# Kernel optimization log

Hardware: AMD Instinct MI355X
Metric: run time of the kernel (lower is better)

## Reference

```python
import jax, jax.numpy as jnp
import numpy as np

DIM = 1024
NUM_HEADS = 16
HEAD_DIM = DIM // NUM_HEADS


def _rope_tables(seq_len, dim, dtype):
    # matches llama_rotary_embedding: inv_freq over even indices of head_dim
    inv_freq = 1.0 / (10000.0 ** (jnp.arange(0, dim, 2, dtype=jnp.float32) / dim))
    t = jnp.arange(seq_len, dtype=jnp.float32)
    freqs = jnp.outer(t, inv_freq)  # [S, dim/2]
    return jnp.cos(freqs).astype(dtype), jnp.sin(freqs).astype(dtype)


def _apply_rope(x, cos_emb, sin_emb):
    # x: [B, H, S, hd]; takes interleaved halves, concatenates rotated halves
    x1 = x[..., 0::2]
    x2 = x[..., 1::2]
    return jnp.concatenate((x1 * cos_emb - x2 * sin_emb,
                            x1 * sin_emb + x2 * cos_emb), axis=-1)


def setup_inputs() -> dict:
    key = jax.random.key(0)
    k_x, k_qkv, k_out, k_b = jax.random.split(key, 4)
    B, S, D = 2, 2048, DIM
    x = jax.random.normal(k_x, (B, S, D), dtype=jnp.float32)
    # torch nn.Linear weights are [out_features, in_features]
    w_qkv = jax.random.normal(k_qkv, (3 * D, D), dtype=jnp.float32) * (1.0 / np.sqrt(D))
    w_out = jax.random.normal(k_out, (D, D), dtype=jnp.float32) * (1.0 / np.sqrt(D))
    b_out = jax.random.normal(k_b, (D,), dtype=jnp.float32) * 0.01
    return {"x": x, "w_qkv": w_qkv, "w_out": w_out, "b_out": b_out}


def reference(x, w_qkv, w_out, b_out):
    B, S, D = x.shape
    H, hd = NUM_HEADS, HEAD_DIM
    qkv = jnp.einsum('bsd,ed->bse', x, w_qkv)  # [B, S, 3D]
    q, k, v = jnp.split(qkv, 3, axis=-1)
    # [B, S, D] -> [B, H, S, hd]
    q, k, v = (t.reshape(B, S, H, hd).transpose(0, 2, 1, 3) for t in (q, k, v))
    cos_emb, sin_emb = _rope_tables(S, hd, x.dtype)  # [S, hd/2]
    q = _apply_rope(q, cos_emb, sin_emb)
    k = _apply_rope(k, cos_emb, sin_emb)
    scores = jnp.einsum('bhqd,bhkd->bhqk', q, k) / jnp.sqrt(jnp.asarray(hd, x.dtype))
    attn = jax.nn.softmax(scores, axis=-1)
    out = jnp.einsum('bhqk,bhkd->bhqd', attn, v)
    out = out.transpose(0, 2, 1, 3).reshape(B, S, D)
    return jnp.einsum('bsd,ed->bse', out, w_out) + b_out
```

## Files before the change

### kernel.cpp

```cpp
#include <hip/hip_runtime.h>
#include <math.h>

typedef __bf16 bf16_t;
typedef bf16_t bf16x8 __attribute__((ext_vector_type(8)));
typedef bf16_t bf16x4 __attribute__((ext_vector_type(4)));
typedef short  s16x4  __attribute__((ext_vector_type(4)));
typedef float  f32x4  __attribute__((ext_vector_type(4)));

#define DIM_   1024
#define NHEADS 16
#define HDIM   64
#define SEQ    2048
#define BATCH  2

#define QK_SCALE 0.18033688011112042f

__device__ __forceinline__ s16x4 as_s16x4(bf16x4 v) {
    union { bf16x4 b; s16x4 s; } u; u.b = v; return u.s;
}

__device__ __forceinline__ void gld16(const bf16_t* g, bf16_t* l) {
    __builtin_amdgcn_global_load_lds(
        (const __attribute__((address_space(1))) void*)g,
        (__attribute__((address_space(3))) void*)l, 16, 0, 0);
}

#define XCNT   (4096u * 1024u)
#define WQCNT  (3072u * 1024u)
#define WOCNT  (1024u * 1024u)
__global__ __launch_bounds__(256) void cast3(const float* __restrict__ s0,
                                             const float* __restrict__ s1,
                                             const float* __restrict__ s2,
                                             bf16_t* __restrict__ d0,
                                             bf16_t* __restrict__ d1,
                                             bf16_t* __restrict__ d2) {
    size_t i = ((size_t)blockIdx.x * 256 + threadIdx.x) * 8;
    const float* s; bf16_t* d; size_t off;
    if (i < XCNT)               { s = s0; d = d0; off = i; }
    else if (i < XCNT + WQCNT)  { s = s1; d = d1; off = i - XCNT; }
    else                        { s = s2; d = d2; off = i - XCNT - WQCNT; }
    float4 a = *(const float4*)(s + off);
    float4 b = *(const float4*)(s + off + 4);
    bf16x8 o = { (bf16_t)a.x, (bf16_t)a.y, (bf16_t)a.z, (bf16_t)a.w,
                 (bf16_t)b.x, (bf16_t)b.y, (bf16_t)b.z, (bf16_t)b.w };
    *(bf16x8*)(d + off) = o;
}

template <bool QKV>
__global__ __launch_bounds__(256) void gemm_lds(const bf16_t* __restrict__ A,
                                                const bf16_t* __restrict__ B,
                                                const float* __restrict__ bias,
                                                void* __restrict__ Cout,
                                                bf16_t* __restrict__ vt,
                                                int M, int N, int K) {
    __shared__ __align__(16) bf16_t As[128 * 32];
    __shared__ __align__(16) bf16_t Bs[128 * 32];
    const int tid  = threadIdx.x;
    const int m0   = blockIdx.y * 128;
    const int n0   = blockIdx.x * 128;
    const int w    = tid >> 6;
    const int lane = tid & 63;
    const int m16  = lane & 15;
    const int quad = lane >> 4;
    const int wm   = (w >> 1) * 64;
    const int wn   = (w & 1) * 64;
    const int lrow = lane >> 2;
    const int lcol = (lane & 3) * 8;

    const bf16_t* pa0 = A + (size_t)(m0 + w * 16 + lrow) * K + lcol;
    const bf16_t* pb0 = B + (size_t)(n0 + w * 16 + lrow) * K + lcol;
    bf16_t* lA0 = &As[(w * 16) * 32];
    bf16_t* lA1 = &As[(64 + w * 16) * 32];
    bf16_t* lB0 = &Bs[(w * 16) * 32];
    bf16_t* lB1 = &Bs[(64 + w * 16) * 32];

    f32x4 acc[4][4] = {};

    for (int k0 = 0; k0 < K; k0 += 32) {
        __syncthreads();
        gld16(pa0 + k0, lA0);
        gld16(pa0 + (size_t)64 * K + k0, lA1);
        gld16(pb0 + k0, lB0);
        gld16(pb0 + (size_t)64 * K + k0, lB1);
        __syncthreads();

        bf16x8 af[4], bfr[4];
#pragma unroll
        for (int i = 0; i < 4; ++i)
            af[i] = *(const bf16x8*)(&As[(wm + i * 16 + m16) * 32 + quad * 8]);
#pragma unroll
        for (int j = 0; j < 4; ++j)
            bfr[j] = *(const bf16x8*)(&Bs[(wn + j * 16 + m16) * 32 + quad * 8]);
#pragma unroll
        for (int i = 0; i < 4; ++i)
#pragma unroll
            for (int j = 0; j < 4; ++j)
                acc[i][j] = __builtin_amdgcn_mfma_f32_16x16x32_bf16(af[i], bfr[j], acc[i][j], 0, 0, 0);
    }

    if (QKV && n0 >= 2 * DIM_) {
        const int b      = m0 >> 11;
        const int s_base = (m0 & (SEQ - 1)) + wm;
#pragma unroll
        for (int j = 0; j < 4; ++j) {
            const int cit = wn + j * 16 + m16;
            const int h   = ((n0 - 2 * DIM_) >> 6) + (cit >> 6);
            const int d   = cit & 63;
            bf16_t* vrow = vt + ((size_t)(b * 16 + h) * 64 + d) * SEQ + s_base;
#pragma unroll
            for (int i = 0; i < 4; ++i) {
                bf16x4 ov = { (bf16_t)acc[i][j][0], (bf16_t)acc[i][j][1],
                              (bf16_t)acc[i][j][2], (bf16_t)acc[i][j][3] };
                *(bf16x4*)(vrow + i * 16 + quad * 4) = ov;
            }
        }
    } else if (QKV) {
        bf16_t* C = (bf16_t*)Cout;
#pragma unroll
        for (int i = 0; i < 4; ++i)
#pragma unroll
            for (int j = 0; j < 4; ++j) {
                const int col = n0 + wn + j * 16 + m16;
#pragma unroll
                for (int r = 0; r < 4; ++r)
                    C[(size_t)(m0 + wm + i * 16 + quad * 4 + r) * N + col] = (bf16_t)acc[i][j][r];
            }
    } else {
        float* C = (float*)Cout;
#pragma unroll
        for (int j = 0; j < 4; ++j) {
            const int col = n0 + wn + j * 16 + m16;
            const float bv = bias[col];
#pragma unroll
            for (int i = 0; i < 4; ++i)
#pragma unroll
                for (int r = 0; r < 4; ++r)
                    C[(size_t)(m0 + wm + i * 16 + quad * 4 + r) * N + col] = acc[i][j][r] + bv;
        }
    }
}

__global__ __launch_bounds__(256) void rope_bf16(bf16_t* __restrict__ qkv) {
    __shared__ float ctab[8][32];
    __shared__ float stab[8][32];
    const int tid = threadIdx.x;
    const int sl  = tid >> 5, j = tid & 31;
    const int s   = (int)((blockIdx.x * 8 + sl) & (SEQ - 1));
    const float freq = exp2f(-0.41524101186092029f * (float)j);
    float sn, cs;
    sincosf((float)s * freq, &sn, &cs);
    ctab[sl][j] = cs;
    stab[sl][j] = sn;
    __syncthreads();

    const int gid   = blockIdx.x * 256 + tid;
    const int m     = gid >> 5;
    const int rr    = gid & 31;
    const int which = rr >> 4;
    const int hh    = rr & 15;
    const float osc = (which == 0) ? QK_SCALE : 1.0f;

    bf16_t* p = qkv + (size_t)m * (3 * DIM_) + which * DIM_ + hh * HDIM;
    union { bf16_t e[64]; bf16x8 v[8]; } X, O;
#pragma unroll
    for (int i = 0; i < 8; ++i) X.v[i] = *(const bf16x8*)(p + i * 8);
#pragma unroll
    for (int t = 0; t < 32; ++t) {
        const float x1 = (float)X.e[2 * t];
        const float x2 = (float)X.e[2 * t + 1];
        const float c  = ctab[sl][t];
        const float s2 = stab[sl][t];
        O.e[t]      = (bf16_t)((x1 * c - x2 * s2) * osc);
        O.e[32 + t] = (bf16_t)((x1 * s2 + x2 * c) * osc);
    }
#pragma unroll
    for (int i = 0; i < 8; ++i) *(bf16x8*)(p + i * 8) = O.v[i];
}

__global__ __launch_bounds__(256) void attn_mfma(const bf16_t* __restrict__ qkv,
                                                 const bf16_t* __restrict__ vt,
                                                 bf16_t* __restrict__ out) {
    __shared__ __align__(16) char smem[18432];
    bf16_t* Ks   = (bf16_t*)smem;
    bf16_t* Vt   = (bf16_t*)(smem + 9216);
    float*  Ored = (float*)smem;
    float*  Lred = (float*)(smem + 16640);

    const int tid  = threadIdx.x;
    const int w    = tid >> 6;
    const int lane = tid & 63;
    const int m16  = lane & 15;
    const int quad = lane >> 4;
    const int bh   = blockIdx.y;
    const int b    = bh >> 4;
    const int hh   = bh & 15;
    const int q0   = blockIdx.x * 64;

    const size_t rs = 3 * DIM_;
    const bf16_t* qbase = qkv + (size_t)(b * SEQ) * rs + hh * HDIM;
    const bf16_t* kbase = qbase + DIM_;
    const bf16_t* vtg   = vt + (size_t)bh * 64 * SEQ;

    bf16x8 qf[4][2];
#pragma unroll
    for (int n = 0; n < 4; ++n)
#pragma unroll
        for (int kt = 0; kt < 2; ++kt)
            qf[n][kt] = *(const bf16x8*)(qbase + (size_t)(q0 + n * 16 + m16) * rs + kt * 32 + quad * 8);

    f32x4 o[4][4] = {};
    float lp[4] = {};

    const int srow = tid >> 3;
    const int sc8  = (tid & 7) * 8;

    for (int k0 = 0; k0 < SEQ; k0 += 64) {
#pragma unroll
        for (int p = 0; p < 2; ++p) {
            const int row = srow + p * 32;
            *(bf16x8*)(&Ks[row * 72 + sc8]) =
                *(const bf16x8*)(kbase + (size_t)(k0 + row) * rs + sc8);
            *(bf16x8*)(&Vt[row * 72 + sc8]) =
                *(const bf16x8*)(vtg + (size_t)row * SEQ + k0 + sc8);
        }
        __syncthreads();

        bf16x8 ak[2];
#pragma unroll
        for (int kt = 0; kt < 2; ++kt)
            ak[kt] = *(const bf16x8*)(&Ks[(w * 16 + m16) * 72 + kt * 32 + quad * 8]);

        bf16x4 va[4];
#pragma unroll
        for (int ds = 0; ds < 4; ++ds)
            va[ds] = *(const bf16x4*)(&Vt[(ds * 16 + m16) * 72 + w * 16 + quad * 4]);

        s16x4 pb[4];
#pragma unroll
        for (int n = 0; n < 4; ++n) {
            f32x4 c = {};
#pragma unroll
            for (int kt = 0; kt < 2; ++kt)
                c = __builtin_amdgcn_mfma_f32_16x16x32_bf16(ak[kt], qf[n][kt], c, 0, 0, 0);
            bf16x4 pv;
#pragma unroll
            for (int r = 0; r < 4; ++r) {
                const float p = __builtin_amdgcn_exp2f(c[r]);
                lp[n] += p;
                pv[r] = (bf16_t)p;
            }
            pb[n] = as_s16x4(pv);
        }

#pragma unroll
        for (int ds = 0; ds < 4; ++ds)
#pragma unroll
            for (int n = 0; n < 4; ++n)
                o[ds][n] = __builtin_amdgcn_mfma_f32_16x16x16bf16_1k(as_s16x4(va[ds]), pb[n], o[ds][n], 0, 0, 0);
        __syncthreads();
    }

#pragma unroll
    for (int n = 0; n < 4; ++n) {
        lp[n] += __shfl_xor(lp[n], 16);
        lp[n] += __shfl_xor(lp[n], 32);
    }
    if (quad == 0) {
#pragma unroll
        for (int n = 0; n < 4; ++n) Lred[w * 64 + n * 16 + m16] = lp[n];
    }
    __syncthreads();
    const float linv = 1.0f / (Lred[lane] + Lred[64 + lane] + Lred[128 + lane] + Lred[192 + lane]);

    const size_t obase = (size_t)(b * SEQ + q0 + lane) * DIM_ + hh * HDIM;
#pragma unroll
    for (int p = 0; p < 4; ++p) {
        __syncthreads();
#pragma unroll
        for (int n = 0; n < 4; ++n)
#pragma unroll
            for (int r = 0; r < 4; ++r)
                Ored[w * 1040 + (quad * 4 + r) * 65 + n * 16 + m16] = o[p][n][r];
        __syncthreads();
        if (w == p) {
            union { bf16_t e[16]; bf16x8 v[2]; } ob;
#pragma unroll
            for (int d = 0; d < 16; ++d) {
                const float v = Ored[d * 65 + lane] + Ored[1040 + d * 65 + lane] +
                                Ored[2080 + d * 65 + lane] + Ored[3120 + d * 65 + lane];
                ob.e[d] = (bf16_t)(v * linv);
            }
            *(bf16x8*)(out + obase + p * 16)     = ob.v[0];
            *(bf16x8*)(out + obase + p * 16 + 8) = ob.v[1];
        }
    }
}

extern "C" void kernel_launch(void* const* d_in, const int* in_sizes, int n_in,
                              void* d_out, int out_size, void* d_ws, size_t ws_size,
                              hipStream_t stream) {
    const float* x     = (const float*)d_in[0];
    const float* w_qkv = (const float*)d_in[1];
    const float* w_out = (const float*)d_in[2];
    const float* b_out = (const float*)d_in[3];
    float* out = (float*)d_out;

    const int M = BATCH * SEQ;

    bf16_t* qkv_b  = (bf16_t*)d_ws;
    bf16_t* attn_b = qkv_b + (size_t)M * 3 * DIM_;
    bf16_t* vt_b   = attn_b + (size_t)M * DIM_;
    bf16_t* xb     = vt_b + (size_t)BATCH * NHEADS * HDIM * SEQ;
    bf16_t* wqkvb  = xb + (size_t)M * DIM_;
    bf16_t* woutb  = wqkvb + (size_t)3 * DIM_ * DIM_;

    cast3<<<(XCNT + WQCNT + WOCNT) / (256 * 8), 256, 0, stream>>>(
        x, w_qkv, w_out, xb, wqkvb, woutb);

    gemm_lds<true><<<dim3(3 * DIM_ / 128, M / 128), 256, 0, stream>>>(
        xb, wqkvb, nullptr, qkv_b, vt_b, M, 3 * DIM_, DIM_);

    rope_bf16<<<(M * 2 * NHEADS) / 256, 256, 0, stream>>>(qkv_b);

    attn_mfma<<<dim3(SEQ / 64, BATCH * NHEADS), 256, 0, stream>>>(qkv_b, vt_b, attn_b);

    gemm_lds<false><<<dim3(DIM_ / 128, M / 128), 256, 0, stream>>>(
        attn_b, woutb, b_out, out, nullptr, M, DIM_, DIM_);
}
```

Measured before the change: 230.5 us.

## Load K/V fragments directly from global with register prefetch, drop LDS staging

The attention kernel no longer stages K and V^T tiles through shared memory with barriers each iteration. Each wave now loads its own MFMA fragments straight from global memory and prefetches the next tile's fragments into registers while computing the current one. This removes the LDS round trips and the two __syncthreads per key block. In exchange, global loads are less coalesced (strided per-row fragment loads), register pressure goes up, and the wrapped prefetch on the last iteration issues a redundant load.

```diff
diff --git a/kernel.cpp b/kernel.cpp
--- a/kernel.cpp
+++ b/kernel.cpp
@@ -180,11 +180,8 @@
 __global__ __launch_bounds__(256) void attn_mfma(const bf16_t* __restrict__ qkv,
                                                  const bf16_t* __restrict__ vt,
                                                  bf16_t* __restrict__ out) {
-    __shared__ __align__(16) char smem[18432];
-    bf16_t* Ks   = (bf16_t*)smem;
-    bf16_t* Vt   = (bf16_t*)(smem + 9216);
-    float*  Ored = (float*)smem;
-    float*  Lred = (float*)(smem + 16640);
+    __shared__ float Ored[4 * 16 * 65];
+    __shared__ float Lred[256];
 
     const int tid  = threadIdx.x;
     const int w    = tid >> 6;
@@ -198,8 +195,8 @@
 
     const size_t rs = 3 * DIM_;
     const bf16_t* qbase = qkv + (size_t)(b * SEQ) * rs + hh * HDIM;
-    const bf16_t* kbase = qbase + DIM_;
-    const bf16_t* vtg   = vt + (size_t)bh * 64 * SEQ;
+    const bf16_t* kp = qbase + DIM_ + (size_t)(w * 16 + m16) * rs + quad * 8;
+    const bf16_t* vp = vt + ((size_t)bh * 64 + m16) * SEQ + w * 16 + quad * 4;
 
     bf16x8 qf[4][2];
 #pragma unroll
@@ -211,37 +208,31 @@
     f32x4 o[4][4] = {};
     float lp[4] = {};
 
-    const int srow = tid >> 3;
-    const int sc8  = (tid & 7) * 8;
-
-    for (int k0 = 0; k0 < SEQ; k0 += 64) {
-#pragma unroll
-        for (int p = 0; p < 2; ++p) {
-            const int row = srow + p * 32;
-            *(bf16x8*)(&Ks[row * 72 + sc8]) =
-                *(const bf16x8*)(kbase + (size_t)(k0 + row) * rs + sc8);
-            *(bf16x8*)(&Vt[row * 72 + sc8]) =
-                *(const bf16x8*)(vtg + (size_t)row * SEQ + k0 + sc8);
-        }
-        __syncthreads();
-
-        bf16x8 ak[2];
-#pragma unroll
-        for (int kt = 0; kt < 2; ++kt)
-            ak[kt] = *(const bf16x8*)(&Ks[(w * 16 + m16) * 72 + kt * 32 + quad * 8]);
-
-        bf16x4 va[4];
+    bf16x8 ka[2];
+    bf16x4 va[4];
+    ka[0] = *(const bf16x8*)(kp);
+    ka[1] = *(const bf16x8*)(kp + 32);
+#pragma unroll
+    for (int ds = 0; ds < 4; ++ds)
+        va[ds] = *(const bf16x4*)(vp + (size_t)ds * 16 * SEQ);
+
+#pragma unroll 2
+    for (int t = 0; t < 32; ++t) {
+        const int tn = (t + 1) & 31;
+        bf16x8 kn[2];
+        bf16x4 vn[4];
+        kn[0] = *(const bf16x8*)(kp + (size_t)tn * 64 * rs);
+        kn[1] = *(const bf16x8*)(kp + (size_t)tn * 64 * rs + 32);
 #pragma unroll
         for (int ds = 0; ds < 4; ++ds)
-            va[ds] = *(const bf16x4*)(&Vt[(ds * 16 + m16) * 72 + w * 16 + quad * 4]);
+            vn[ds] = *(const bf16x4*)(vp + (size_t)ds * 16 * SEQ + tn * 64);
 
         s16x4 pb[4];
 #pragma unroll
         for (int n = 0; n < 4; ++n) {
             f32x4 c = {};
-#pragma unroll
-            for (int kt = 0; kt < 2; ++kt)
-                c = __builtin_amdgcn_mfma_f32_16x16x32_bf16(ak[kt], qf[n][kt], c, 0, 0, 0);
+            c = __builtin_amdgcn_mfma_f32_16x16x32_bf16(ka[0], qf[n][0], c, 0, 0, 0);
+            c = __builtin_amdgcn_mfma_f32_16x16x32_bf16(ka[1], qf[n][1], c, 0, 0, 0);
             bf16x4 pv;
 #pragma unroll
             for (int r = 0; r < 4; ++r) {
@@ -257,7 +248,10 @@
 #pragma unroll
             for (int n = 0; n < 4; ++n)
                 o[ds][n] = __builtin_amdgcn_mfma_f32_16x16x16bf16_1k(as_s16x4(va[ds]), pb[n], o[ds][n], 0, 0, 0);
-        __syncthreads();
+
+        ka[0] = kn[0]; ka[1] = kn[1];
+#pragma unroll
+        for (int ds = 0; ds < 4; ++ds) va[ds] = vn[ds];
     }
 
 #pragma unroll
```

Result: slower. 251.7 us (+9.2%).

## Give each wave private double-buffered K/V tiles and drop per-tile block barriers

Applied to the files above, without the earlier changes.

Each wave now loads only the 16 K rows and matching V^T columns it consumes into its own double-buffered LDS region. The global loads for the next tile are issued into registers before computing the current tile and written to the other buffer afterwards. Because no wave reads another wave's data, the two __syncthreads per key tile go away, and global latency is overlapped with MFMA work. In exchange, LDS use grows from about 18 KB to about 39 KB, which may limit blocks per CU. Holding the prefetched tile in registers also adds register pressure.

```diff
diff --git a/kernel.cpp b/kernel.cpp
--- a/kernel.cpp
+++ b/kernel.cpp
@@ -180,9 +180,9 @@
 __global__ __launch_bounds__(256) void attn_mfma(const bf16_t* __restrict__ qkv,
                                                  const bf16_t* __restrict__ vt,
                                                  bf16_t* __restrict__ out) {
-    __shared__ __align__(16) char smem[18432];
-    bf16_t* Ks   = (bf16_t*)smem;
-    bf16_t* Vt   = (bf16_t*)(smem + 9216);
+    __shared__ __align__(16) char smem[39936];
+    bf16_t* KW   = (bf16_t*)smem;
+    bf16_t* VW   = (bf16_t*)(smem + 18432);
     float*  Ored = (float*)smem;
     float*  Lred = (float*)(smem + 16640);
 
@@ -198,8 +198,20 @@
 
     const size_t rs = 3 * DIM_;
     const bf16_t* qbase = qkv + (size_t)(b * SEQ) * rs + hh * HDIM;
-    const bf16_t* kbase = qbase + DIM_;
     const bf16_t* vtg   = vt + (size_t)bh * 64 * SEQ;
+
+    const int krow = lane >> 2;
+    const int kcol = (lane & 3) << 4;
+    const bf16_t* kg = qbase + DIM_ + (size_t)(w * 16 + krow) * rs + kcol;
+    const bf16_t* vg = vtg + (size_t)lane * SEQ + w * 16;
+    bf16_t* kl[2] = { &KW[(w * 2 + 0) * 1152 + krow * 72 + kcol],
+                      &KW[(w * 2 + 1) * 1152 + krow * 72 + kcol] };
+    bf16_t* vl[2] = { &VW[(w * 2 + 0) * 1280 + lane * 20],
+                      &VW[(w * 2 + 1) * 1280 + lane * 20] };
+    const bf16_t* kf[2] = { &KW[(w * 2 + 0) * 1152 + m16 * 72 + quad * 8],
+                            &KW[(w * 2 + 1) * 1152 + m16 * 72 + quad * 8] };
+    const bf16_t* vf[2] = { &VW[(w * 2 + 0) * 1280 + m16 * 20 + quad * 4],
+                            &VW[(w * 2 + 1) * 1280 + m16 * 20 + quad * 4] };
 
     bf16x8 qf[4][2];
 #pragma unroll
@@ -211,37 +223,28 @@
     f32x4 o[4][4] = {};
     float lp[4] = {};
 
-    const int srow = tid >> 3;
-    const int sc8  = (tid & 7) * 8;
-
-    for (int k0 = 0; k0 < SEQ; k0 += 64) {
-#pragma unroll
-        for (int p = 0; p < 2; ++p) {
-            const int row = srow + p * 32;
-            *(bf16x8*)(&Ks[row * 72 + sc8]) =
-                *(const bf16x8*)(kbase + (size_t)(k0 + row) * rs + sc8);
-            *(bf16x8*)(&Vt[row * 72 + sc8]) =
-                *(const bf16x8*)(vtg + (size_t)row * SEQ + k0 + sc8);
-        }
-        __syncthreads();
-
-        bf16x8 ak[2];
-#pragma unroll
-        for (int kt = 0; kt < 2; ++kt)
-            ak[kt] = *(const bf16x8*)(&Ks[(w * 16 + m16) * 72 + kt * 32 + quad * 8]);
-
+    bf16x8 kr0 = *(const bf16x8*)(kg);
+    bf16x8 kr1 = *(const bf16x8*)(kg + 8);
+    bf16x8 vr0 = *(const bf16x8*)(vg);
+    bf16x8 vr1 = *(const bf16x8*)(vg + 8);
+    *(bf16x8*)(kl[0])     = kr0;
+    *(bf16x8*)(kl[0] + 8) = kr1;
+    *(bf16x8*)(vl[0])     = vr0;
+    *(bf16x8*)(vl[0] + 8) = vr1;
+
+    auto compute_tile = [&](int buf) {
+        bf16x8 ak0 = *(const bf16x8*)(kf[buf]);
+        bf16x8 ak1 = *(const bf16x8*)(kf[buf] + 32);
         bf16x4 va[4];
 #pragma unroll
         for (int ds = 0; ds < 4; ++ds)
-            va[ds] = *(const bf16x4*)(&Vt[(ds * 16 + m16) * 72 + w * 16 + quad * 4]);
-
+            va[ds] = *(const bf16x4*)(vf[buf] + ds * 16 * 20);
         s16x4 pb[4];
 #pragma unroll
         for (int n = 0; n < 4; ++n) {
             f32x4 c = {};
-#pragma unroll
-            for (int kt = 0; kt < 2; ++kt)
-                c = __builtin_amdgcn_mfma_f32_16x16x32_bf16(ak[kt], qf[n][kt], c, 0, 0, 0);
+            c = __builtin_amdgcn_mfma_f32_16x16x32_bf16(ak0, qf[n][0], c, 0, 0, 0);
+            c = __builtin_amdgcn_mfma_f32_16x16x32_bf16(ak1, qf[n][1], c, 0, 0, 0);
             bf16x4 pv;
 #pragma unroll
             for (int r = 0; r < 4; ++r) {
@@ -251,20 +254,37 @@
             }
             pb[n] = as_s16x4(pv);
         }
-
 #pragma unroll
         for (int ds = 0; ds < 4; ++ds)
 #pragma unroll
             for (int n = 0; n < 4; ++n)
                 o[ds][n] = __builtin_amdgcn_mfma_f32_16x16x16bf16_1k(as_s16x4(va[ds]), pb[n], o[ds][n], 0, 0, 0);
-        __syncthreads();
-    }
+    };
+
+    for (int t = 0; t < 31; ++t) {
+        kg += (size_t)64 * rs;
+        vg += 64;
+        kr0 = *(const bf16x8*)(kg);
+        kr1 = *(const bf16x8*)(kg + 8);
+        vr0 = *(const bf16x8*)(vg);
+        vr1 = *(const bf16x8*)(vg + 8);
+
+        compute_tile(t & 1);
+
+        const int nb = (t + 1) & 1;
+        *(bf16x8*)(kl[nb])     = kr0;
+        *(bf16x8*)(kl[nb] + 8) = kr1;
+        *(bf16x8*)(vl[nb])     = vr0;
+        *(bf16x8*)(vl[nb] + 8) = vr1;
+    }
+    compute_tile(1);
 
 #pragma unroll
     for (int n = 0; n < 4; ++n) {
         lp[n] += __shfl_xor(lp[n], 16);
         lp[n] += __shfl_xor(lp[n], 32);
     }
+    __syncthreads();
     if (quad == 0) {
 #pragma unroll
         for (int n = 0; n < 4; ++n) Lred[w * 64 + n * 16 + m16] = lp[n];
```

New measurement: 252.1 us. 1.09x slower.
